# Optimization experiments

Hardware: AMD Instinct MI355X
Metric: run time of the kernel (lower is better)

The kernel has to match this reference:

```python
import jax, jax.numpy as jnp
import numpy as np

B, DX, DY, H, T, L = 256, 256, 256, 512, 128, 2
EPS = 1e-5


def setup_inputs() -> dict:
    key = jax.random.key(0)
    ks = jax.random.split(key, 16)
    s = 0.02
    return {
        "inputx": jax.random.normal(ks[0], (B, DX, T), dtype=jnp.float32),
        "inputy": jax.random.normal(ks[1], (B, DY, T), dtype=jnp.float32),
        # stacked gate weights: f,i,o for T-path and F-path, [L, 3H, Dx+Dy+H]
        "WTg": jax.random.normal(ks[2], (L, 3 * H, DX + DY + H), dtype=jnp.float32) * s,
        "bTg": jax.random.normal(ks[3], (L, 3 * H), dtype=jnp.float32) * s,
        "WFg": jax.random.normal(ks[4], (L, 3 * H, DX + DY + H), dtype=jnp.float32) * s,
        "bFg": jax.random.normal(ks[5], (L, 3 * H), dtype=jnp.float32) * s,
        # candidate cell weights
        "WTc": jax.random.normal(ks[6], (L, H, DX + H), dtype=jnp.float32) * s,
        "bTc": jax.random.normal(ks[7], (L, H), dtype=jnp.float32) * s,
        "WFc": jax.random.normal(ks[8], (L, H, DY + H), dtype=jnp.float32) * s,
        "bFc": jax.random.normal(ks[9], (L, H), dtype=jnp.float32) * s,
        # batchnorm affine params per layer
        "gammaT": jnp.ones((L, H), dtype=jnp.float32),
        "betaT": jnp.zeros((L, H), dtype=jnp.float32),
        "gammaF": jnp.ones((L, H), dtype=jnp.float32),
        "betaF": jnp.zeros((L, H), dtype=jnp.float32),
    }


def _batchnorm(h, gamma, beta):
    # train-mode BN over batch dim, biased variance (torch semantics)
    mu = jnp.mean(h, axis=0, keepdims=True)
    var = jnp.mean((h - mu) ** 2, axis=0, keepdims=True)
    return (h - mu) * jax.lax.rsqrt(var + EPS) * gamma + beta


def _forward(inputx, inputy, WTg, bTg, WFg, bFg, WTc, bTc, WFc, bFc,
             gammaT, betaT, gammaF, betaF):
    nL = WTg.shape[0]
    b, h = inputx.shape[0], gammaT.shape[1]
    zeros = jnp.zeros((nL, b, h), dtype=inputx.dtype)

    def step(carry, xy):
        hT, hF, CT, CF = carry  # each [L, B, H]
        x, y = xy  # [B, Dx], [B, Dy]
        hT_n, hF_n, CT_n, CF_n = [], [], [], []
        for i in range(nL):
            catT = jnp.concatenate([x, y, hT[i]], axis=1)
            catF = jnp.concatenate([x, y, hF[i]], axis=1)
            gT = jax.nn.sigmoid(catT @ WTg[i].T + bTg[i])  # [B, 3H]
            gF = jax.nn.sigmoid(catF @ WFg[i].T + bFg[i])
            fT, iT, oT = jnp.split(gT, 3, axis=1)
            fF, iF, oF = jnp.split(gF, 3, axis=1)
            cT = jnp.tanh(jnp.concatenate([x, hT[i]], axis=1) @ WTc[i].T + bTc[i])
            cF = jnp.tanh(jnp.concatenate([y, hF[i]], axis=1) @ WFc[i].T + bFc[i])
            CTi = fT * CT[i] + iT * cT
            CFi = fF * CF[i] + iF * cF
            hTi = oT * jnp.tanh(CTi)
            hFi = oF * jnp.tanh(CFi)
            hT_n.append(hTi); hF_n.append(hFi); CT_n.append(CTi); CF_n.append(CFi)
        hT = jnp.stack(hT_n); hF = jnp.stack(hF_n)
        CT = jnp.stack(CT_n); CF = jnp.stack(CF_n)
        # output comes from last layer only; BN in train mode
        outT = _batchnorm(hT[-1], gammaT[-1], betaT[-1])
        outF = _batchnorm(hF[-1], gammaF[-1], betaF[-1])
        return (hT, hF, CT, CF), (outT, outF)

    xs = (jnp.transpose(inputx, (2, 0, 1)), jnp.transpose(inputy, (2, 0, 1)))
    _, (outT_seq, outF_seq) = jax.lax.scan(step, (zeros, zeros, zeros, zeros), xs)
    # [T, B, H] -> [B, H, T] (torch.stack(..., dim=2))
    return jnp.transpose(outT_seq, (1, 2, 0)), jnp.transpose(outF_seq, (1, 2, 0))


def reference(inputx, inputy, WTg, bTg, WFg, bFg, WTc, bTc, WFc, bFc,
              gammaT, betaT, gammaF, betaF):
    return _forward(inputx, inputy, WTg, bTg, WFg, bFg, WTc, bTc, WFc, bFc,
                    gammaT, betaT, gammaF, betaF)
```

## Files before the change

kernel.cpp:

```cpp
#include <hip/hip_runtime.h>

#define NBLK 256
#define NTHR 512

typedef __attribute__((ext_vector_type(8))) short s16x8;
typedef __attribute__((ext_vector_type(8))) __bf16 bf16x8;
typedef __attribute__((ext_vector_type(4))) float f32x4;

__device__ __forceinline__ ushort f2bf(float f) {
  uint u = __float_as_uint(f);
  return (ushort)((u + 0x7FFFu + ((u >> 16) & 1u)) >> 16);
}
__device__ __forceinline__ float bf2f(ushort s) {
  return __uint_as_float(((uint)s) << 16);
}
__device__ __forceinline__ float sigm(float x) { return 1.f / (1.f + __expf(-x)); }
__device__ __forceinline__ float tanhf_(float x) {
  x = fminf(9.f, fmaxf(-9.f, x));
  float e = __expf(2.f * x);
  return (e - 1.f) / (e + 1.f);
}

#define MFMA(a, b, c) __builtin_amdgcn_mfma_f32_16x16x32_bf16( \
    __builtin_bit_cast(bf16x8, a), __builtin_bit_cast(bf16x8, b), c, 0, 0, 0)

__global__ void init_k(uint* __restrict__ bar) {
  int i = blockIdx.x * blockDim.x + threadIdx.x;
  if (i < 512) bar[i] = 0u;
}

__global__ void xyt_k(const float* __restrict__ x, const float* __restrict__ y,
                      ushort* __restrict__ xyT) {
  __shared__ ushort sT[64 * 130];
  const int bid = blockIdx.x;
  const int chunk = bid & 7;
  const int b = bid >> 3;
  const int d0 = (chunk & 3) * 64;
  const float* src = ((chunk < 4) ? x : y) + ((size_t)b * 256 + d0) * 128;
  const int tid = threadIdx.x;
  const int tt = tid & 127, rr = tid >> 7;
#pragma unroll
  for (int i = 0; i < 32; ++i) {
    int row = i * 2 + rr;
    sT[row * 130 + tt] = f2bf(src[(size_t)row * 128 + tt]);
  }
  __syncthreads();
  const int dbase = ((chunk < 4) ? 0 : 256) + d0;
#pragma unroll
  for (int i = 0; i < 16; ++i) {
    int idx = tid + i * 256;
    int t = idx >> 5, j = idx & 31;
    uint v = (uint)sT[(2 * j) * 130 + t] | ((uint)sT[(2 * j + 1) * 130 + t] << 16);
    *(uint*)(xyT + ((size_t)t * 256 + b) * 512 + dbase + 2 * j) = v;
  }
}

__launch_bounds__(NTHR, 2)
__global__ void seq_k(const ushort* __restrict__ xyT,
                      ushort* __restrict__ hist,
                      const float* __restrict__ WTg, const float* __restrict__ WFg,
                      const float* __restrict__ WTc, const float* __restrict__ WFc,
                      const float* __restrict__ bTg, const float* __restrict__ bFg,
                      const float* __restrict__ bTc, const float* __restrict__ bFc,
                      uint* bar) {
  extern __shared__ char smem[];
  float* sAcc = (float*)(smem + 98304);

  const int tid = threadIdx.x;
  const int bid = blockIdx.x;
  const int mt = bid & 7;
  const int cg = (bid >> 3) & 15;
  const int s = bid >> 7;
  const int g = s * 8 + mt;
  const int m0 = mt * 32;
  const int j0 = cg * 32;
  const int w = tid >> 6;
  const int l = tid & 63;
  const int l15 = l & 15;
  const int q16 = (l >> 4) * 16;
  const bool isGate = (w < 6);
  const int kh = w & 1;
  uint* fl = bar + (g << 4);

  s16x8 wreg[2][16];
  if (isGate) {
    const int gt = w >> 1;
#pragma unroll
    for (int p = 0; p < 2; ++p) {
      const float* Wrow = ((s == 0) ? WTg : WFg) + 1572864
                        + ((size_t)(gt * 512 + j0 + p * 16 + l15)) * 1024 + (q16 >> 1);
#pragma unroll
      for (int kk = 0; kk < 8; ++kk) {
        s16x8 v;
#pragma unroll
        for (int e = 0; e < 8; ++e) v[e] = (short)f2bf(Wrow[kh * 256 + kk * 32 + e]);
        wreg[p][kk] = v;
      }
#pragma unroll
      for (int kk = 0; kk < 8; ++kk) {
        s16x8 v;
#pragma unroll
        for (int e = 0; e < 8; ++e) v[e] = (short)f2bf(Wrow[512 + kh * 256 + kk * 32 + e]);
        wreg[p][8 + kk] = v;
      }
    }
  } else {
#pragma unroll
    for (int p = 0; p < 2; ++p) {
      const float* Wrow = ((s == 0) ? WTc : WFc) + 393216
                        + ((size_t)(j0 + p * 16 + l15)) * 768 + (q16 >> 1);
#pragma unroll
      for (int kk = 0; kk < 4; ++kk) {
        s16x8 v;
#pragma unroll
        for (int e = 0; e < 8; ++e) v[e] = (short)f2bf(Wrow[kh * 128 + kk * 32 + e]);
        wreg[p][kk] = v;
      }
#pragma unroll
      for (int kk = 0; kk < 8; ++kk) {
        s16x8 v;
#pragma unroll
        for (int e = 0; e < 8; ++e) v[e] = (short)f2bf(Wrow[256 + kh * 256 + kk * 32 + e]);
        wreg[p][4 + kk] = v;
      }
    }
  }

  const int ro = tid >> 4;
  const int cc0 = (tid & 15) * 2;
  float bfv0, bfv1, biv0, biv1, bov0, bov1, bcv0, bcv1;
  {
    const float* bg = ((s == 0) ? bTg : bFg) + 1536;
    const float* bc = ((s == 0) ? bTc : bFc) + 512;
    int col = j0 + cc0;
    bfv0 = bg[col];        bfv1 = bg[col + 1];
    biv0 = bg[512 + col];  biv1 = bg[513 + col];
    bov0 = bg[1024 + col]; bov1 = bg[1025 + col];
    bcv0 = bc[col];        bcv1 = bc[col + 1];
  }
  float C0 = 0.f, C1 = 0.f;

  auto stage_row = [&](const ushort* gbase, char* lbase, int r) {
    const char* srow = (const char*)(gbase + (size_t)r * 512);
    int off = (l * 16) ^ ((r & 7) << 4);
    __builtin_amdgcn_global_load_lds(
        (const __attribute__((address_space(1))) void*)(srow + off),
        (__attribute__((address_space(3))) void*)(lbase + (r << 10)), 16, 0, 0);
  };
  auto stage_row_coh = [&](const ushort* gbase, char* lbase, int r) {
    const char* srow = (const char*)(gbase + (size_t)r * 512);
    int off = (l * 16) ^ ((r & 7) << 4);
    __builtin_amdgcn_global_load_lds(
        (const __attribute__((address_space(1))) void*)(srow + off),
        (__attribute__((address_space(3))) void*)(lbase + (r << 10)), 16, 0, 17);
  };

  {
#pragma unroll
    for (int i = 0; i < 4; ++i) stage_row(xyT + (size_t)m0 * 512, smem, (w << 2) + i);
  }
  __syncthreads();

  const int sw = (l15 & 7) << 4;
  for (int t = 0; t < 128; ++t) {
    const int cur = t & 1;
    char* xyb = smem + cur * 32768;
    char* xybn = smem + (cur ^ 1) * 32768;
    char* hb = smem + 65536;

    f32x4 acc00 = {0.f, 0.f, 0.f, 0.f};
    f32x4 acc01 = {0.f, 0.f, 0.f, 0.f};
    f32x4 acc10 = {0.f, 0.f, 0.f, 0.f};
    f32x4 acc11 = {0.f, 0.f, 0.f, 0.f};

    {
      const char* base0 = xyb + (l15 << 10);
      const char* base1 = xyb + ((16 + l15) << 10);
      if (isGate) {
#pragma unroll
        for (int kk = 0; kk < 8; ++kk) {
          int c2 = (kh * 512 + kk * 64 + q16) ^ sw;
          s16x8 a0 = *(const s16x8*)(base0 + c2);
          s16x8 a1 = *(const s16x8*)(base1 + c2);
          acc00 = MFMA(a0, wreg[0][kk], acc00);
          acc01 = MFMA(a1, wreg[0][kk], acc01);
          acc10 = MFMA(a0, wreg[1][kk], acc10);
          acc11 = MFMA(a1, wreg[1][kk], acc11);
        }
      } else {
#pragma unroll
        for (int kk = 0; kk < 4; ++kk) {
          int c2 = (s * 512 + kh * 256 + kk * 64 + q16) ^ sw;
          s16x8 a0 = *(const s16x8*)(base0 + c2);
          s16x8 a1 = *(const s16x8*)(base1 + c2);
          acc00 = MFMA(a0, wreg[0][kk], acc00);
          acc01 = MFMA(a1, wreg[0][kk], acc01);
          acc10 = MFMA(a0, wreg[1][kk], acc10);
          acc11 = MFMA(a1, wreg[1][kk], acc11);
        }
      }
    }

    if (w == 0 && t) {
      const uint tgt = (uint)t;
      while (true) {
        uint v = (l < 16)
                     ? __hip_atomic_load(fl + l, __ATOMIC_RELAXED, __HIP_MEMORY_SCOPE_SYSTEM)
                     : tgt;
        if (__all((int)(v >= tgt))) break;
        __builtin_amdgcn_s_sleep(1);
      }
    }
    __builtin_amdgcn_s_barrier();

    if (t) {
      const ushort* hsrc = hist + (((size_t)s * 128 + (t - 1)) * 256 + m0) * 512;
#pragma unroll
      for (int i = 0; i < 4; ++i) stage_row_coh(hsrc, hb, (w << 2) + i);
    }
    {
      const int tn = (t < 127) ? t + 1 : 127;
      const ushort* xyNext = xyT + ((size_t)(tn * 256 + m0)) * 512;
#pragma unroll
      for (int i = 0; i < 4; ++i) stage_row(xyNext, xybn, (w << 2) + i);
    }

    asm volatile("s_waitcnt vmcnt(4)" ::: "memory");
    __builtin_amdgcn_sched_barrier(0);
    __builtin_amdgcn_s_barrier();
    __builtin_amdgcn_sched_barrier(0);

    if (t) {
      const char* base0 = hb + (l15 << 10);
      const char* base1 = hb + ((16 + l15) << 10);
      if (isGate) {
#pragma unroll
        for (int kk = 0; kk < 8; ++kk) {
          int c2 = (kh * 512 + kk * 64 + q16) ^ sw;
          s16x8 a0 = *(const s16x8*)(base0 + c2);
          s16x8 a1 = *(const s16x8*)(base1 + c2);
          acc00 = MFMA(a0, wreg[0][8 + kk], acc00);
          acc01 = MFMA(a1, wreg[0][8 + kk], acc01);
          acc10 = MFMA(a0, wreg[1][8 + kk], acc10);
          acc11 = MFMA(a1, wreg[1][8 + kk], acc11);
        }
      } else {
#pragma unroll
        for (int kk = 0; kk < 8; ++kk) {
          int c2 = (kh * 512 + kk * 64 + q16) ^ sw;
          s16x8 a0 = *(const s16x8*)(base0 + c2);
          s16x8 a1 = *(const s16x8*)(base1 + c2);
          acc00 = MFMA(a0, wreg[0][4 + kk], acc00);
          acc01 = MFMA(a1, wreg[0][4 + kk], acc01);
          acc10 = MFMA(a0, wreg[1][4 + kk], acc10);
          acc11 = MFMA(a1, wreg[1][4 + kk], acc11);
        }
      }
    }

    {
      float* sl = sAcc + w * 1088 + l15;
      const int r0 = q16 >> 2;
#pragma unroll
      for (int rg = 0; rg < 4; ++rg) {
        sl[(r0 + rg) * 34] = acc00[rg];
        sl[(16 + r0 + rg) * 34] = acc01[rg];
        sl[(r0 + rg) * 34 + 16] = acc10[rg];
        sl[(16 + r0 + rg) * 34 + 16] = acc11[rg];
      }
    }
    asm volatile("s_waitcnt lgkmcnt(0)" ::: "memory");
    __builtin_amdgcn_sched_barrier(0);
    __builtin_amdgcn_s_barrier();
    __builtin_amdgcn_sched_barrier(0);

    {
      const int eb = ro * 34 + cc0;
      float2 f0v = *(const float2*)&sAcc[eb];
      float2 f1v = *(const float2*)&sAcc[1088 + eb];
      float2 i0v = *(const float2*)&sAcc[2176 + eb];
      float2 i1v = *(const float2*)&sAcc[3264 + eb];
      float2 o0v = *(const float2*)&sAcc[4352 + eb];
      float2 o1v = *(const float2*)&sAcc[5440 + eb];
      float2 c0v = *(const float2*)&sAcc[6528 + eb];
      float2 c1v = *(const float2*)&sAcc[7616 + eb];
      float f0 = sigm(f0v.x + f1v.x + bfv0), f1 = sigm(f0v.y + f1v.y + bfv1);
      float i0 = sigm(i0v.x + i1v.x + biv0), i1 = sigm(i0v.y + i1v.y + biv1);
      float o0 = sigm(o0v.x + o1v.x + bov0), o1 = sigm(o0v.y + o1v.y + bov1);
      float c0 = tanhf_(c0v.x + c1v.x + bcv0), c1 = tanhf_(c0v.y + c1v.y + bcv1);
      C0 = f0 * C0 + i0 * c0;
      C1 = f1 * C1 + i1 * c1;
      float h0 = o0 * tanhf_(C0);
      float h1 = o1 * tanhf_(C1);
      uint hp = (uint)f2bf(h0) | (((uint)f2bf(h1)) << 16);
      __hip_atomic_store(
          (uint*)(hist + (((size_t)s * 128 + t) * 256 + m0 + ro) * 512 + j0 + cc0), hp,
          __ATOMIC_RELAXED, __HIP_MEMORY_SCOPE_SYSTEM);
    }
    __syncthreads();
    if (tid == 0)
      __hip_atomic_store(fl + cg, (uint)(t + 1), __ATOMIC_RELAXED, __HIP_MEMORY_SCOPE_SYSTEM);
  }
}

__global__ void bnstat_k(const ushort* __restrict__ hist,
                         const float* __restrict__ gT, const float* __restrict__ beT,
                         const float* __restrict__ gF, const float* __restrict__ beF,
                         float* __restrict__ scale, float* __restrict__ shift) {
  const int t = blockIdx.x >> 1, s = blockIdx.x & 1;
  const int tid = threadIdx.x;
  const ushort* hp = hist + ((size_t)s * 128 + t) * 256 * 512;
  const float* gp = (s ? gF : gT) + 512;
  const float* bp = (s ? beF : beT) + 512;
#pragma unroll
  for (int hh = 0; hh < 2; ++hh) {
    const int h = tid + hh * 256;
    float sum = 0.f, sq = 0.f;
#pragma unroll 8
    for (int b = 0; b < 256; ++b) {
      float v = bf2f(hp[(size_t)b * 512 + h]);
      sum += v;
      sq += v * v;
    }
    float mu = sum * 0.00390625f;
    float var = sq * 0.00390625f - mu * mu;
    float sc = (1.0f / sqrtf(var + 1e-5f)) * gp[h];
    size_t o = ((size_t)s * 128 + t) * 512 + h;
    scale[o] = sc;
    shift[o] = bp[h] - mu * sc;
  }
}

__global__ void bnwrite_k(const ushort* __restrict__ hist, const float* __restrict__ scale,
                          const float* __restrict__ shift, float* __restrict__ out) {
  __shared__ float sT[64 * 129];
  const int bid = blockIdx.x;
  const int hc = bid & 7, b = (bid >> 3) & 255, s = bid >> 11;
  const int h0 = hc * 64;
  const int tid = threadIdx.x;
  const int hh = tid & 63, tq = tid >> 6;
#pragma unroll 4
  for (int tc = 0; tc < 32; ++tc) {
    const int t = tc * 4 + tq;
    const size_t so = ((size_t)s * 128 + t) * 512 + h0 + hh;
    float v = bf2f(hist[(((size_t)s * 128 + t) * 256 + b) * 512 + h0 + hh]);
    sT[hh * 129 + t] = v * scale[so] + shift[so];
  }
  __syncthreads();
  const int t2 = tid & 127, hq = tid >> 7;
#pragma unroll 4
  for (int i = 0; i < 32; ++i) {
    const int h = i * 2 + hq;
    out[(size_t)s * 16777216 + ((size_t)b * 512 + h0 + h) * 128 + t2] = sT[h * 129 + t2];
  }
}

extern "C" void kernel_launch(void* const* d_in, const int* in_sizes, int n_in,
                              void* d_out, int out_size, void* d_ws, size_t ws_size,
                              hipStream_t stream) {
  const float* inputx = (const float*)d_in[0];
  const float* inputy = (const float*)d_in[1];
  const float* WTg = (const float*)d_in[2];
  const float* bTg = (const float*)d_in[3];
  const float* WFg = (const float*)d_in[4];
  const float* bFg = (const float*)d_in[5];
  const float* WTc = (const float*)d_in[6];
  const float* bTc = (const float*)d_in[7];
  const float* WFc = (const float*)d_in[8];
  const float* bFc = (const float*)d_in[9];
  const float* gT = (const float*)d_in[10];
  const float* beT = (const float*)d_in[11];
  const float* gF = (const float*)d_in[12];
  const float* beF = (const float*)d_in[13];
  float* out = (float*)d_out;

  char* ws = (char*)d_ws;
  ushort* xyT = (ushort*)ws;
  ushort* hist = (ushort*)(ws + 34603008);
  float* scale = (float*)(ws + 101711872);
  float* shift = (float*)(ws + 102236160);
  uint* bar = (uint*)(ws + 102760448);

  init_k<<<2, 256, 0, stream>>>(bar);
  xyt_k<<<2048, 256, 0, stream>>>(inputx, inputy, xyT);

  hipFuncSetAttribute((const void*)seq_k, hipFuncAttributeMaxDynamicSharedMemorySize, 133120);
  void* args[11];
  args[0] = &xyT; args[1] = &hist;
  args[2] = &WTg; args[3] = &WFg; args[4] = &WTc; args[5] = &WFc;
  args[6] = &bTg; args[7] = &bFg; args[8] = &bTc; args[9] = &bFc;
  args[10] = &bar;
  hipLaunchCooperativeKernel((const void*)seq_k, dim3(NBLK), dim3(NTHR), args, 133120, stream);

  bnstat_k<<<256, 256, 0, stream>>>(hist, gT, beT, gF, beF, scale, shift);
  bnwrite_k<<<4096, 256, 0, stream>>>(hist, scale, shift, out);
}
```

Before: 545.7 us.

## Load recurrent hidden state directly into registers, bypassing LDS staging

The previous-step hidden state is now read straight from global memory into registers with coherent (sc0 sc1) dwordx4 loads, and these feed the MFMAs directly. Before, it was staged through LDS with a barrier round-trip. The flag wait now runs at the top of each step, so these loads overlap the x/y MFMA work. Prefetch of the next x/y tile moves to after the accumulator stores, and dynamic LDS shrinks because the hidden-state buffer is gone. The trade-offs are higher register pressure from 16 vector loads per lane, and the x/y MFMA phase can no longer hide the flag-wait latency, since the wait now comes first.

```diff
diff --git a/kernel.cpp b/kernel.cpp
--- a/kernel.cpp
+++ b/kernel.cpp
@@ -23,6 +23,13 @@
 
 #define MFMA(a, b, c) __builtin_amdgcn_mfma_f32_16x16x32_bf16( \
     __builtin_bit_cast(bf16x8, a), __builtin_bit_cast(bf16x8, b), c, 0, 0, 0)
+
+__device__ __forceinline__ s16x8 gload_coh(const char* p) {
+  s16x8 r;
+  asm volatile("global_load_dwordx4 %0, %1, off sc0 sc1"
+               : "=v"(r) : "v"(p) : "memory");
+  return r;
+}
 
 __global__ void init_k(uint* __restrict__ bar) {
   int i = blockIdx.x * blockDim.x + threadIdx.x;
@@ -64,7 +71,7 @@
                       const float* __restrict__ bTc, const float* __restrict__ bFc,
                       uint* bar) {
   extern __shared__ char smem[];
-  float* sAcc = (float*)(smem + 98304);
+  float* sAcc = (float*)(smem + 65536);
 
   const int tid = threadIdx.x;
   const int bid = blockIdx.x;
@@ -147,13 +154,6 @@
         (const __attribute__((address_space(1))) void*)(srow + off),
         (__attribute__((address_space(3))) void*)(lbase + (r << 10)), 16, 0, 0);
   };
-  auto stage_row_coh = [&](const ushort* gbase, char* lbase, int r) {
-    const char* srow = (const char*)(gbase + (size_t)r * 512);
-    int off = (l * 16) ^ ((r & 7) << 4);
-    __builtin_amdgcn_global_load_lds(
-        (const __attribute__((address_space(1))) void*)(srow + off),
-        (__attribute__((address_space(3))) void*)(lbase + (r << 10)), 16, 0, 17);
-  };
 
   {
 #pragma unroll
@@ -166,7 +166,30 @@
     const int cur = t & 1;
     char* xyb = smem + cur * 32768;
     char* xybn = smem + (cur ^ 1) * 32768;
-    char* hb = smem + 65536;
+
+    if (w == 0 && t) {
+      const uint tgt = (uint)t;
+      while (true) {
+        uint v = (l < 16)
+                     ? __hip_atomic_load(fl + l, __ATOMIC_RELAXED, __HIP_MEMORY_SCOPE_SYSTEM)
+                     : tgt;
+        if (__all((int)(v >= tgt))) break;
+        __builtin_amdgcn_s_sleep(1);
+      }
+    }
+    __builtin_amdgcn_s_barrier();
+
+    s16x8 ha0[8], ha1[8];
+    if (t) {
+      const char* h0p = (const char*)(hist + (((size_t)s * 128 + (t - 1)) * 256 + m0 + l15) * 512)
+                        + kh * 512 + q16;
+      const char* h1p = h0p + (16 << 10);
+#pragma unroll
+      for (int kk = 0; kk < 8; ++kk) {
+        ha0[kk] = gload_coh(h0p + kk * 64);
+        ha1[kk] = gload_coh(h1p + kk * 64);
+      }
+    }
 
     f32x4 acc00 = {0.f, 0.f, 0.f, 0.f};
     f32x4 acc01 = {0.f, 0.f, 0.f, 0.f};
@@ -201,59 +224,26 @@
       }
     }
 
-    if (w == 0 && t) {
-      const uint tgt = (uint)t;
-      while (true) {
-        uint v = (l < 16)
-                     ? __hip_atomic_load(fl + l, __ATOMIC_RELAXED, __HIP_MEMORY_SCOPE_SYSTEM)
-                     : tgt;
-        if (__all((int)(v >= tgt))) break;
-        __builtin_amdgcn_s_sleep(1);
-      }
-    }
-    __builtin_amdgcn_s_barrier();
+    __builtin_amdgcn_sched_barrier(0);
+    asm volatile("s_waitcnt vmcnt(0)" ::: "memory");
+    __builtin_amdgcn_sched_barrier(0);
 
     if (t) {
-      const ushort* hsrc = hist + (((size_t)s * 128 + (t - 1)) * 256 + m0) * 512;
-#pragma unroll
-      for (int i = 0; i < 4; ++i) stage_row_coh(hsrc, hb, (w << 2) + i);
-    }
-    {
-      const int tn = (t < 127) ? t + 1 : 127;
-      const ushort* xyNext = xyT + ((size_t)(tn * 256 + m0)) * 512;
-#pragma unroll
-      for (int i = 0; i < 4; ++i) stage_row(xyNext, xybn, (w << 2) + i);
-    }
-
-    asm volatile("s_waitcnt vmcnt(4)" ::: "memory");
-    __builtin_amdgcn_sched_barrier(0);
-    __builtin_amdgcn_s_barrier();
-    __builtin_amdgcn_sched_barrier(0);
-
-    if (t) {
-      const char* base0 = hb + (l15 << 10);
-      const char* base1 = hb + ((16 + l15) << 10);
       if (isGate) {
 #pragma unroll
         for (int kk = 0; kk < 8; ++kk) {
-          int c2 = (kh * 512 + kk * 64 + q16) ^ sw;
-          s16x8 a0 = *(const s16x8*)(base0 + c2);
-          s16x8 a1 = *(const s16x8*)(base1 + c2);
-          acc00 = MFMA(a0, wreg[0][8 + kk], acc00);
-          acc01 = MFMA(a1, wreg[0][8 + kk], acc01);
-          acc10 = MFMA(a0, wreg[1][8 + kk], acc10);
-          acc11 = MFMA(a1, wreg[1][8 + kk], acc11);
+          acc00 = MFMA(ha0[kk], wreg[0][8 + kk], acc00);
+          acc01 = MFMA(ha1[kk], wreg[0][8 + kk], acc01);
+          acc10 = MFMA(ha0[kk], wreg[1][8 + kk], acc10);
+          acc11 = MFMA(ha1[kk], wreg[1][8 + kk], acc11);
         }
       } else {
 #pragma unroll
         for (int kk = 0; kk < 8; ++kk) {
-          int c2 = (kh * 512 + kk * 64 + q16) ^ sw;
-          s16x8 a0 = *(const s16x8*)(base0 + c2);
-          s16x8 a1 = *(const s16x8*)(base1 + c2);
-          acc00 = MFMA(a0, wreg[0][4 + kk], acc00);
-          acc01 = MFMA(a1, wreg[0][4 + kk], acc01);
-          acc10 = MFMA(a0, wreg[1][4 + kk], acc10);
-          acc11 = MFMA(a1, wreg[1][4 + kk], acc11);
+          acc00 = MFMA(ha0[kk], wreg[0][4 + kk], acc00);
+          acc01 = MFMA(ha1[kk], wreg[0][4 + kk], acc01);
+          acc10 = MFMA(ha0[kk], wreg[1][4 + kk], acc10);
+          acc11 = MFMA(ha1[kk], wreg[1][4 + kk], acc11);
         }
       }
     }
@@ -269,6 +259,15 @@
         sl[(16 + r0 + rg) * 34 + 16] = acc11[rg];
       }
     }
+
+    __builtin_amdgcn_sched_barrier(0);
+    {
+      const int tn = (t < 127) ? t + 1 : 127;
+      const ushort* xyNext = xyT + ((size_t)(tn * 256 + m0)) * 512;
+#pragma unroll
+      for (int i = 0; i < 4; ++i) stage_row(xyNext, xybn, (w << 2) + i);
+    }
+
     asm volatile("s_waitcnt lgkmcnt(0)" ::: "memory");
     __builtin_amdgcn_sched_barrier(0);
     __builtin_amdgcn_s_barrier();
@@ -384,13 +383,13 @@
   init_k<<<2, 256, 0, stream>>>(bar);
   xyt_k<<<2048, 256, 0, stream>>>(inputx, inputy, xyT);
 
-  hipFuncSetAttribute((const void*)seq_k, hipFuncAttributeMaxDynamicSharedMemorySize, 133120);
+  hipFuncSetAttribute((const void*)seq_k, hipFuncAttributeMaxDynamicSharedMemorySize, 100352);
   void* args[11];
   args[0] = &xyT; args[1] = &hist;
   args[2] = &WTg; args[3] = &WFg; args[4] = &WTc; args[5] = &WFc;
   args[6] = &bTg; args[7] = &bFg; args[8] = &bTc; args[9] = &bFc;
   args[10] = &bar;
-  hipLaunchCooperativeKernel((const void*)seq_k, dim3(NBLK), dim3(NTHR), args, 133120, stream);
+  hipLaunchCooperativeKernel((const void*)seq_k, dim3(NBLK), dim3(NTHR), args, 100352, stream);
 
   bnstat_k<<<256, 256, 0, stream>>>(hist, gT, beT, gF, beF, scale, shift);
   bnwrite_k<<<4096, 256, 0, stream>>>(hist, scale, shift, out);
```

Result: slower. 1.041 ms (+90.8%).
